# Optimization experiments

Measured on AMD Instinct MI355X. Metric: run time of the kernel, lower is better.

The kernel has to match this reference:

```python
import jax, jax.numpy as jnp
import numpy as np
import math

EPS_NORM = 1e-6
EPS_COS = 1e-6
B, L, LC = 2, 2048, 1024
D_MODEL, D_CROSS, D_HEAD = 1024, 1024, 64
N_HEADS = D_MODEL // D_HEAD


def setup_inputs() -> dict:
    key = jax.random.key(0)
    ks = jax.random.split(key, 6)
    x = jax.random.normal(ks[0], (B, L, D_MODEL), jnp.float32)
    pos = jax.random.uniform(ks[1], (B, L, 2), dtype=jnp.float32)  # normalized 2D canvas coords
    x_cross = jax.random.normal(ks[2], (B, LC, D_CROSS), jnp.float32)
    norm_scale = jnp.ones((D_MODEL,), jnp.float32)          # RMSNorm scale (init ones)
    norm_cross_scale = jnp.ones((D_CROSS,), jnp.float32)
    q_w = jax.random.normal(ks[3], (D_MODEL, D_MODEL), jnp.float32) / math.sqrt(D_MODEL)
    kv_w = jax.random.normal(ks[4], (D_CROSS, 2 * D_MODEL), jnp.float32) / math.sqrt(D_CROSS)
    # out_proj is zero-init in the original; use small random weights so the block is non-trivial
    out_w = jax.random.normal(ks[5], (D_MODEL, D_MODEL), jnp.float32) / math.sqrt(D_MODEL)
    scale = jnp.full((N_HEADS,), 10.0, jnp.float32)          # learned per-head cosine-sim scale
    # AxialRoPE2D freqs (k-diffusion style, learnable_freqs=False): [n_heads, d_head//4]
    log_min, log_max = math.log(math.pi), math.log(10.0 * math.pi)
    freqs = jnp.exp(jnp.linspace(log_min, log_max, N_HEADS * D_HEAD // 4 + 1)[:-1])
    freqs = freqs.reshape(D_HEAD // 4, N_HEADS).T            # [H, E//4]
    return dict(x=x, pos=pos, x_cross=x_cross, norm_scale=norm_scale,
                norm_cross_scale=norm_cross_scale, q_w=q_w, kv_w=kv_w,
                scale=scale, out_w=out_w, freqs=freqs)


def _rms_norm(x, scale, eps=EPS_NORM):
    ms = jnp.mean(jnp.square(x), axis=-1, keepdims=True)
    return x * (scale * jax.lax.rsqrt(ms + eps))


def reference(x, pos, x_cross, norm_scale, norm_cross_scale, q_w, kv_w, scale, out_w, freqs):
    skip = x
    xn = _rms_norm(x, norm_scale)
    xc = _rms_norm(x_cross, norm_cross_scale)
    q = xn @ q_w                                             # [B,L,D]
    kv = xc @ kv_w                                           # [B,LC,2D]
    q = q.reshape(B, L, N_HEADS, D_HEAD).transpose(0, 2, 1, 3)      # [B,H,L,E]
    kv = kv.reshape(B, LC, 2, N_HEADS, D_HEAD)               # split (t nh e), t outermost
    k = kv[:, :, 0].transpose(0, 2, 1, 3)                    # [B,H,LC,E]
    v = kv[:, :, 1].transpose(0, 2, 1, 3)
    # per-head cosine-sim QK scaling
    sq = jnp.sqrt(scale)[:, None, None]                      # [H,1,1]
    q = q * (sq * jax.lax.rsqrt(jnp.sum(jnp.square(q), -1, keepdims=True) + EPS_COS))
    k = k * (sq * jax.lax.rsqrt(jnp.sum(jnp.square(k), -1, keepdims=True) + EPS_COS))
    # axial 2D RoPE on q only (as in the original forward)
    theta = jnp.concatenate([pos[..., None, 0:1] * freqs,
                             pos[..., None, 1:2] * freqs], -1)      # [B,L,H,E//2]
    theta = jnp.moveaxis(theta, -2, -3)                      # [B,H,L,E//2]
    d = theta.shape[-1]
    q1, q2 = q[..., :d], q[..., d:]
    cos, sin = jnp.cos(theta), jnp.sin(theta)
    q = jnp.concatenate([q1 * cos - q2 * sin, q2 * cos + q1 * sin], -1)
    # SDPA with scale=1.0 (cosine-sim scaling already applied)
    attn = jax.nn.softmax(jnp.einsum('bhqe,bhke->bhqk', q, k), axis=-1)
    o = jnp.einsum('bhqk,bhke->bhqe', attn, v)
    o = o.transpose(0, 2, 1, 3).reshape(B, L, D_MODEL)       # merge heads
    return o @ out_w + skip
```

## Files before the change

kernel.cpp:

```cpp
#include <hip/hip_runtime.h>
#include <math.h>

typedef unsigned short u16;
typedef __bf16 bf16x8 __attribute__((ext_vector_type(8)));
typedef float f32x4 __attribute__((ext_vector_type(4)));

#define EPS_NORM 1e-6f
#define EPS_COS  1e-6f

static constexpr int Bc = 2;
static constexpr int Lq = 2048;
static constexpr int Lc = 1024;
static constexpr int Dm = 1024;
static constexpr int DH = 64;
static constexpr int NH = 16;

#define F32MODE(probe) ((probe)[0] == 0x3F800000u)

__device__ __forceinline__ float b2f(u16 u) {
  union { unsigned u; float f; } x; x.u = ((unsigned)u) << 16; return x.f;
}
__device__ __forceinline__ u16 f2b(float f) {
  union { float f; unsigned u; } x; x.f = f;
  unsigned v = x.u;
  v += 0x7fffu + ((v >> 16) & 1u);
  return (u16)(v >> 16);
}
__device__ __forceinline__ unsigned pkbf(float lo, float hi) {
#if __has_builtin(__builtin_amdgcn_cvt_pk_bf16_f32)
  return __builtin_bit_cast(unsigned, __builtin_amdgcn_cvt_pk_bf16_f32(lo, hi));
#else
  unsigned r;
  asm("v_cvt_pk_bf16_f32 %0, %1, %2" : "=v"(r) : "v"(lo), "v"(hi));
  return r;
#endif
}
__device__ __forceinline__ float ex2(float x) {
#if __has_builtin(__builtin_amdgcn_exp2f)
  return __builtin_amdgcn_exp2f(x);
#else
  return exp2f(x);
#endif
}
__device__ __forceinline__ float loadf(const void* p, size_t i, bool f32m) {
  return f32m ? ((const float*)p)[i] : b2f(((const u16*)p)[i]);
}
__device__ __forceinline__ void gll16(const u16* g, u16* l) {
  __builtin_amdgcn_global_load_lds(
      (const __attribute__((address_space(1))) unsigned*)g,
      (__attribute__((address_space(3))) unsigned*)l, 16, 0, 0);
}

__global__ __launch_bounds__(256) void prep_kernel(
    const void* __restrict__ qw, const void* __restrict__ kvw,
    const void* __restrict__ outw, u16* __restrict__ wqw,
    u16* __restrict__ wkvw, u16* __restrict__ woutw,
    const void* __restrict__ x, const void* __restrict__ xcr,
    const void* __restrict__ nsc, const void* __restrict__ ncs,
    u16* __restrict__ xn, u16* __restrict__ xc,
    const unsigned* __restrict__ probe) {
  bool f32m = F32MODE(probe);
  int id = blockIdx.x;
  int t = threadIdx.x;
  if (id < 6144) {
    int row = id;
    const void* src; const void* sc; u16* dst;
    if (row < Bc * Lq) { src = x; sc = nsc; dst = xn; }
    else { row -= Bc * Lq; src = xcr; sc = ncs; dst = xc; }
    float f[4]; float ss = 0.f;
    if (f32m) {
      float4 a = *(const float4*)((const float*)src + (size_t)row * Dm + t * 4);
      f[0] = a.x; f[1] = a.y; f[2] = a.z; f[3] = a.w;
    } else {
      union { uint2 u2; u16 s[4]; } v;
      v.u2 = *(const uint2*)((const u16*)src + (size_t)row * Dm + t * 4);
#pragma unroll
      for (int i = 0; i < 4; i++) f[i] = b2f(v.s[i]);
    }
#pragma unroll
    for (int i = 0; i < 4; i++) ss += f[i] * f[i];
#pragma unroll
    for (int o = 32; o > 0; o >>= 1) ss += __shfl_xor(ss, o, 64);
    __shared__ float red[4];
    if ((t & 63) == 0) red[t >> 6] = ss;
    __syncthreads();
    float inv = rsqrtf((red[0] + red[1] + red[2] + red[3]) / (float)Dm + EPS_NORM);
    union { uint2 u2; u16 s[4]; } ov;
#pragma unroll
    for (int i = 0; i < 4; i++) ov.s[i] = f2b(f[i] * loadf(sc, t * 4 + i, f32m) * inv);
    *(uint2*)(dst + (size_t)row * Dm + t * 4) = ov.u2;
  } else {
    id -= 6144;
    __shared__ u16 tile[32][33];
    const void* src; u16* dst; int N;
    if (id < 1024)      { src = qw;   dst = wqw;   N = Dm; }
    else if (id < 3072) { src = kvw;  dst = wkvw;  N = 2 * Dm; id -= 1024; }
    else                { src = outw; dst = woutw; N = Dm;     id -= 3072; }
    int k0 = (id & 31) * 32, n0 = (id >> 5) * 32;
    int tn = t & 31, tg = t >> 5;
#pragma unroll
    for (int r = 0; r < 4; r++) {
      int k = tg * 4 + r;
      tile[k][tn] = f2b(loadf(src, (size_t)(k0 + k) * N + n0 + tn, f32m));
    }
    __syncthreads();
#pragma unroll
    for (int r = 0; r < 4; r++) {
      int n = tg * 4 + r;
      dst[(size_t)(n0 + n) * Dm + k0 + tn] = tile[tn][n];
    }
  }
}

__device__ __forceinline__ void gemm_body(
    const u16* __restrict__ A, const u16* __restrict__ Bt,
    int M, int N, int m0, int n0, int mode,
    u16* __restrict__ outb, u16* __restrict__ kfp, u16* __restrict__ vt,
    const void* __restrict__ skip, void* __restrict__ Cn,
    const void* __restrict__ scale, const void* __restrict__ pos,
    const void* __restrict__ freqs, bool f32m,
    u16 (&As)[2][8192], u16 (&Bs)[2][4096]) {
  constexpr int K = Dm;
  int t = threadIdx.x;
  int wv = t >> 6, lane = t & 63;
  int r16 = lane & 15, quad = lane >> 4;

  const u16* pA[4]; const u16* pB[2]; int iLA[4], iLB[2];
#pragma unroll
  for (int c = 0; c < 4; c++) {
    int i = c * 256 + t;
    int row = i >> 3, g = (i & 7) ^ (row & 7);
    pA[c] = A + (size_t)(m0 + row) * K + g * 8;
    iLA[c] = (c * 256 + wv * 64) * 8;
  }
#pragma unroll
  for (int c = 0; c < 2; c++) {
    int i = c * 256 + t;
    int row = i >> 3, g = (i & 7) ^ (row & 7);
    pB[c] = Bt + (size_t)(n0 + row) * K + g * 8;
    iLB[c] = (c * 256 + wv * 64) * 8;
  }

  int offA[2][2], offB[2][4];
#pragma unroll
  for (int kh = 0; kh < 2; kh++) {
    int pa = ((kh * 4 + quad) ^ (r16 & 7)) * 8;
#pragma unroll
    for (int i = 0; i < 2; i++) offA[kh][i] = (wv * 32 + i * 16 + r16) * 64 + pa;
#pragma unroll
    for (int j = 0; j < 4; j++) offB[kh][j] = (j * 16 + r16) * 64 + pa;
  }

  f32x4 acc[2][4] = {};

#pragma unroll
  for (int c = 0; c < 4; c++) gll16(pA[c], &As[0][iLA[c]]);
#pragma unroll
  for (int c = 0; c < 2; c++) gll16(pB[c], &Bs[0][iLB[c]]);

  int niter = K >> 6;
  for (int it = 0; it < niter; ++it) {
    __syncthreads();
    if (it + 1 < niter) {
      int koff = (it + 1) << 6;
      int nb = (it + 1) & 1;
#pragma unroll
      for (int c = 0; c < 4; c++) gll16(pA[c] + koff, &As[nb][iLA[c]]);
#pragma unroll
      for (int c = 0; c < 2; c++) gll16(pB[c] + koff, &Bs[nb][iLB[c]]);
    }
    const u16* Ab = As[it & 1];
    const u16* Bb = Bs[it & 1];
#pragma unroll
    for (int kh = 0; kh < 2; kh++) {
      bf16x8 af[2], bf[4];
#pragma unroll
      for (int i = 0; i < 2; i++)
        af[i] = __builtin_bit_cast(bf16x8, *(const uint4*)(Ab + offA[kh][i]));
#pragma unroll
      for (int j = 0; j < 4; j++)
        bf[j] = __builtin_bit_cast(bf16x8, *(const uint4*)(Bb + offB[kh][j]));
#pragma unroll
      for (int mt = 0; mt < 2; mt++)
#pragma unroll
        for (int nt = 0; nt < 4; nt++)
          acc[mt][nt] = __builtin_amdgcn_mfma_f32_16x16x32_bf16(
              af[mt], bf[nt], acc[mt][nt], 0, 0, 0);
    }
  }

  if (mode == 2) {
#pragma unroll
    for (int mt = 0; mt < 2; mt++)
#pragma unroll
      for (int nt = 0; nt < 4; nt++)
#pragma unroll
        for (int r = 0; r < 4; r++) {
          int m = m0 + wv * 32 + mt * 16 + quad * 4 + r;
          int n = n0 + nt * 16 + r16;
          size_t idx = (size_t)m * N + n;
          float v = acc[mt][nt][r] + loadf(skip, idx, f32m);
          if (f32m) ((float*)Cn)[idx] = v;
          else      outb[idx] = f2b(v);
        }
    return;
  }

  if (mode == 1 && n0 >= Dm) {
    int hh = (n0 - Dm) >> 6;
#pragma unroll
    for (int mt = 0; mt < 2; mt++)
#pragma unroll
      for (int r = 0; r < 4; r++) {
        int m = m0 + wv * 32 + mt * 16 + quad * 4 + r;
        int bb = m >> 10, lc = m & (Lc - 1);
        u16* tb = vt + ((size_t)(bb * NH + hh) * 16 + (lc >> 6)) * 4096;
        int kin = lc & 63;
#pragma unroll
        for (int nt = 0; nt < 4; nt++) {
          int d = nt * 16 + r16;
          tb[d * 64 + ((kin >> 3) ^ (d & 7)) * 8 + (kin & 7)] = f2b(acc[mt][nt][r]);
        }
      }
    return;
  }

  int hh = (n0 & (Dm - 1)) >> 6;
  float sqs = sqrtf(loadf(scale, hh, f32m));
  float fr = (mode == 0) ? loadf(freqs, hh * 16 + r16, f32m) : 0.f;
#pragma unroll
  for (int mt = 0; mt < 2; mt++) {
    float ss[4];
#pragma unroll
    for (int r = 0; r < 4; r++) {
      ss[r] = 0.f;
#pragma unroll
      for (int nt = 0; nt < 4; nt++) ss[r] += acc[mt][nt][r] * acc[mt][nt][r];
    }
#pragma unroll
    for (int o = 1; o < 16; o <<= 1)
#pragma unroll
      for (int r = 0; r < 4; r++) ss[r] += __shfl_xor(ss[r], o, 64);
#pragma unroll
    for (int r = 0; r < 4; r++) {
      int m = m0 + wv * 32 + mt * 16 + quad * 4 + r;
      float inv = sqs * rsqrtf(ss[r] + EPS_COS);
      if (mode == 1) {
        int bb = m >> 10, lc = m & (Lc - 1);
        size_t base = ((size_t)((bb * NH + hh) * Lc) + lc) * 64;
#pragma unroll
        for (int nt = 0; nt < 4; nt++)
          kfp[base + nt * 16 + r16] = f2b(acc[mt][nt][r] * inv);
      } else {
        int bb = m >> 11, l = m & (Lq - 1);
        float p0 = loadf(pos, (size_t)m * 2 + 0, f32m);
        float p1 = loadf(pos, (size_t)m * 2 + 1, f32m);
        size_t base = ((size_t)((bb * NH + hh) * Lq) + l) * 64;
#pragma unroll
        for (int nt = 0; nt < 2; nt++) {
          float th = (nt ? p1 : p0) * fr;
          float c, s;
          sincosf(th, &s, &c);
          float lo = acc[mt][nt][r] * inv, hi = acc[mt][nt + 2][r] * inv;
          outb[base + nt * 16 + r16]       = f2b(lo * c - hi * s);
          outb[base + (nt + 2) * 16 + r16] = f2b(hi * c + lo * s);
        }
      }
    }
  }
}

__global__ __launch_bounds__(256) void qkv_gemm_kernel(
    const u16* __restrict__ xn, const u16* __restrict__ wqw,
    const u16* __restrict__ xc, const u16* __restrict__ wkvw,
    u16* __restrict__ qf, u16* __restrict__ kf, u16* __restrict__ vt,
    const void* __restrict__ scale, const void* __restrict__ pos,
    const void* __restrict__ freqs, const unsigned* __restrict__ probe) {
  __shared__ u16 As[2][8192];
  __shared__ u16 Bs[2][4096];
  bool f32m = F32MODE(probe);
  int blk = blockIdx.x;
  if (blk < 512) {
    gemm_body(xn, wqw, Bc * Lq, Dm, (blk >> 4) * 128, (blk & 15) * 64, 0,
              qf, nullptr, nullptr, nullptr, nullptr, scale, pos, freqs,
              f32m, As, Bs);
  } else {
    int id = blk - 512;
    gemm_body(xc, wkvw, Bc * Lc, 2 * Dm, (id >> 5) * 128, (id & 31) * 64, 1,
              nullptr, kf, vt, nullptr, nullptr, scale, nullptr, nullptr,
              f32m, As, Bs);
  }
}

__global__ __launch_bounds__(256) void final_gemm_kernel(
    const u16* __restrict__ ob, const u16* __restrict__ woutw,
    const void* __restrict__ skip, void* __restrict__ Cn,
    u16* __restrict__ outb, const unsigned* __restrict__ probe) {
  __shared__ u16 As[2][8192];
  __shared__ u16 Bs[2][4096];
  bool f32m = F32MODE(probe);
  int blk = blockIdx.x;
  gemm_body(ob, woutw, Bc * Lq, Dm, (blk >> 4) * 128, (blk & 15) * 64, 2,
            outb, nullptr, nullptr, skip, Cn, nullptr, nullptr, nullptr,
            f32m, As, Bs);
}

__global__ __launch_bounds__(256) void attn_kernel(
    const u16* __restrict__ qf, const u16* __restrict__ kf,
    const u16* __restrict__ vt, u16* __restrict__ o_out,
    const void* __restrict__ scale, const unsigned* __restrict__ probe) {
  __shared__ u16 Kt[2][4096];
  __shared__ u16 Vs[2][4096];
  __shared__ u16 Pl[4][1024];

  int blk = blockIdx.x;
  int bh = blk & 31;
  int qt = blk >> 5;
  int h = bh & 15;
  bool f32m = F32MODE(probe);
  const float L2E = 1.44269504089f;
  float sh = loadf(scale, h, f32m);
  float shb = sh * L2E;
  const u16* kbase = kf + (size_t)bh * Lc * DH;
  const u16* vtb   = vt + (size_t)bh * 16 * 4096;
  int t = threadIdx.x;
  int wv = t >> 6, lane = t & 63;
  int r16 = lane & 15, quad = lane >> 4;

  const u16* qb0 = qf + ((size_t)bh * Lq + qt * 64 + wv * 16) * DH;
  bf16x8 af00 = __builtin_bit_cast(bf16x8, *(const uint4*)(qb0 + r16 * DH + 0  + quad * 8));
  bf16x8 af01 = __builtin_bit_cast(bf16x8, *(const uint4*)(qb0 + r16 * DH + 32 + quad * 8));

  int e0 = t, e1 = 256 + t;
  int row0 = e0 >> 3, g0 = (e0 & 7) ^ (row0 & 7);
  int row1 = e1 >> 3, g1 = (e1 & 7) ^ (row1 & 7);
  const u16* pK0 = kbase + (size_t)row0 * DH + g0 * 8;
  const u16* pK1 = kbase + (size_t)row1 * DH + g1 * 8;
  const u16* pV0 = vtb + e0 * 8;
  const u16* pV1 = vtb + e1 * 8;
  int iS0 = (wv * 64) * 8, iS1 = (256 + wv * 64) * 8;
  int kphys0 = ((quad)     ^ (r16 & 7)) * 8;
  int kphys1 = ((4 | quad) ^ (r16 & 7)) * 8;

  int poff[4][4];
#pragma unroll
  for (int r = 0; r < 4; r++) {
    int mrow = quad * 4 + r;
    int bx = mrow & 7;
    int base = mrow * 64 + (r16 & 7);
    int c0 = r16 >> 3;
    poff[r][0] = base + ((c0    ) ^ bx) * 8;
    poff[r][1] = base + ((c0 + 2) ^ bx) * 8;
    poff[r][2] = base + ((c0 + 4) ^ bx) * 8;
    poff[r][3] = base + ((c0 + 6) ^ bx) * 8;
  }

  float l0[4] = {0.f, 0.f, 0.f, 0.f};
  f32x4 oa0[4] = {{0,0,0,0},{0,0,0,0},{0,0,0,0},{0,0,0,0}};

  gll16(pK0, &Kt[0][iS0]); gll16(pK1, &Kt[0][iS1]);
  gll16(pV0, &Vs[0][iS0]); gll16(pV1, &Vs[0][iS1]);

  for (int it = 0; it < Lc / 64; ++it) {
    __syncthreads();
    if (it + 1 < Lc / 64) {
      size_t koff = (size_t)(it + 1) * 64 * DH;
      size_t voff = (size_t)(it + 1) * 4096;
      int nb = (it + 1) & 1;
      gll16(pK0 + koff, &Kt[nb][iS0]);
      gll16(pK1 + koff, &Kt[nb][iS1]);
      gll16(pV0 + voff, &Vs[nb][iS0]);
      gll16(pV1 + voff, &Vs[nb][iS1]);
    }
    const u16* Kb = Kt[it & 1];
    const u16* Vb = Vs[it & 1];

    f32x4 s0[4];
#pragma unroll
    for (int nt = 0; nt < 4; nt++) {
      int nrow = (nt * 16 + r16) * 64;
      bf16x8 bf0 = __builtin_bit_cast(bf16x8, *(const uint4*)(Kb + nrow + kphys0));
      bf16x8 bf1 = __builtin_bit_cast(bf16x8, *(const uint4*)(Kb + nrow + kphys1));
      s0[nt] = (f32x4){0.f, 0.f, 0.f, 0.f};
      s0[nt] = __builtin_amdgcn_mfma_f32_16x16x32_bf16(af00, bf0, s0[nt], 0, 0, 0);
      s0[nt] = __builtin_amdgcn_mfma_f32_16x16x32_bf16(af01, bf1, s0[nt], 0, 0, 0);
    }

    {
      u16* P = &Pl[wv][0];
#pragma unroll
      for (int r = 0; r < 4; r++) {
        float p0 = ex2(fmaf(s0[0][r], L2E, -shb));
        float p1 = ex2(fmaf(s0[1][r], L2E, -shb));
        float p2 = ex2(fmaf(s0[2][r], L2E, -shb));
        float p3 = ex2(fmaf(s0[3][r], L2E, -shb));
        l0[r] += (p0 + p1) + (p2 + p3);
        unsigned pa = pkbf(p0, p1), pb = pkbf(p2, p3);
        P[poff[r][0]] = (u16)pa;
        P[poff[r][1]] = (u16)(pa >> 16);
        P[poff[r][2]] = (u16)pb;
        P[poff[r][3]] = (u16)(pb >> 16);
      }
    }

#pragma unroll
    for (int dt = 0; dt < 4; dt++) {
      int vrow = (dt * 16 + r16) * 64;
#pragma unroll
      for (int kc = 0; kc < 2; kc++) {
        int ph = kc ? kphys1 : kphys0;
        bf16x8 bu  = __builtin_bit_cast(bf16x8, *(const uint4*)(Vb + vrow + ph));
        bf16x8 au0 = __builtin_bit_cast(bf16x8, *(const uint4*)&Pl[wv][r16 * 64 + ph]);
        oa0[dt] = __builtin_amdgcn_mfma_f32_16x16x32_bf16(au0, bu, oa0[dt], 0, 0, 0);
      }
    }
  }

  int b = bh >> 4;
  float inv[4];
#pragma unroll
  for (int r = 0; r < 4; r++) {
    float l = l0[r];
#pragma unroll
    for (int o = 8; o > 0; o >>= 1) l += __shfl_xor(l, o, 64);
    inv[r] = 1.f / l;
  }
#pragma unroll
  for (int dt = 0; dt < 4; dt++)
#pragma unroll
    for (int r = 0; r < 4; r++) {
      int m = qt * 64 + wv * 16 + quad * 4 + r;
      o_out[((size_t)(b * Lq + m)) * Dm + h * DH + dt * 16 + r16] =
          f2b(oa0[dt][r] * inv[r]);
    }
}

extern "C" void kernel_launch(void* const* d_in, const int* in_sizes, int n_in,
                              void* d_out, int out_size, void* d_ws, size_t ws_size,
                              hipStream_t stream) {
  const void* x     = d_in[0];
  const void* pos   = d_in[1];
  const void* xcr   = d_in[2];
  const void* nsc   = d_in[3];
  const void* ncs   = d_in[4];
  const void* qw    = d_in[5];
  const void* kvw   = d_in[6];
  const void* scale = d_in[7];
  const void* outw  = d_in[8];
  const void* freqs = d_in[9];
  const unsigned* probe = (const unsigned*)nsc;

  char* ws = (char*)d_ws;
  const size_t MB = 1u << 20;
  u16*   wqw  = (u16*)(ws + 0 * MB);
  u16*   wkvw = (u16*)(ws + 2 * MB);
  u16*   woutw= (u16*)(ws + 6 * MB);
  u16*   xn   = (u16*)(ws + 8 * MB);
  u16*   ob   = (u16*)(ws + 8 * MB);
  u16*   xc   = (u16*)(ws + 16 * MB);
  u16*   qf   = (u16*)(ws + 20 * MB);
  u16*   kf   = (u16*)(ws + 28 * MB);
  u16*   vt   = (u16*)(ws + 32 * MB);

  prep_kernel<<<6144 + 4096, 256, 0, stream>>>(
      qw, kvw, outw, wqw, wkvw, woutw, x, xcr, nsc, ncs, xn, xc, probe);
  qkv_gemm_kernel<<<1024, 256, 0, stream>>>(xn, wqw, xc, wkvw, qf, kf, vt,
                                            scale, pos, freqs, probe);
  attn_kernel<<<1024, 256, 0, stream>>>(qf, kf, vt, ob, scale, probe);
  final_gemm_kernel<<<512, 256, 0, stream>>>(ob, woutw, x, d_out, (u16*)d_out, probe);
}
```

Before: 195.1 us.

## Keep attention probabilities in registers via transposed S MFMA and K row permutation

Computes S^T by swapping MFMA operands so that each lane already holds the probability values in the A-operand layout needed by the PV MFMA. This removes the per-wave LDS scratch buffer and its scattered 16-bit stores and reloads. K rows are permuted at load time so that the register-held P columns line up with the V layout. The row-sum reduction moves to a cross-quad shuffle followed by a broadcast, and correctness depends on the permutation exactly matching the MFMA fragment layout.

```diff
diff --git a/kernel.cpp b/kernel.cpp
--- a/kernel.cpp
+++ b/kernel.cpp
@@ -311,7 +311,6 @@
     const void* __restrict__ scale, const unsigned* __restrict__ probe) {
   __shared__ u16 Kt[2][4096];
   __shared__ u16 Vs[2][4096];
-  __shared__ u16 Pl[4][1024];
 
   int blk = blockIdx.x;
   int bh = blk & 31;
@@ -332,30 +331,19 @@
   bf16x8 af01 = __builtin_bit_cast(bf16x8, *(const uint4*)(qb0 + r16 * DH + 32 + quad * 8));
 
   int e0 = t, e1 = 256 + t;
-  int row0 = e0 >> 3, g0 = (e0 & 7) ^ (row0 & 7);
-  int row1 = e1 >> 3, g1 = (e1 & 7) ^ (row1 & 7);
-  const u16* pK0 = kbase + (size_t)row0 * DH + g0 * 8;
-  const u16* pK1 = kbase + (size_t)row1 * DH + g1 * 8;
+  int rho0 = e0 >> 3, g0 = (e0 & 7) ^ (rho0 & 7);
+  int rho1 = e1 >> 3, g1 = (e1 & 7) ^ (rho1 & 7);
+  int gk0 = ((rho0 & 28) << 1) | ((rho0 & 32) >> 3) | (rho0 & 3);
+  int gk1 = ((rho1 & 28) << 1) | ((rho1 & 32) >> 3) | (rho1 & 3);
+  const u16* pK0 = kbase + (size_t)gk0 * DH + g0 * 8;
+  const u16* pK1 = kbase + (size_t)gk1 * DH + g1 * 8;
   const u16* pV0 = vtb + e0 * 8;
   const u16* pV1 = vtb + e1 * 8;
   int iS0 = (wv * 64) * 8, iS1 = (256 + wv * 64) * 8;
   int kphys0 = ((quad)     ^ (r16 & 7)) * 8;
   int kphys1 = ((4 | quad) ^ (r16 & 7)) * 8;
 
-  int poff[4][4];
-#pragma unroll
-  for (int r = 0; r < 4; r++) {
-    int mrow = quad * 4 + r;
-    int bx = mrow & 7;
-    int base = mrow * 64 + (r16 & 7);
-    int c0 = r16 >> 3;
-    poff[r][0] = base + ((c0    ) ^ bx) * 8;
-    poff[r][1] = base + ((c0 + 2) ^ bx) * 8;
-    poff[r][2] = base + ((c0 + 4) ^ bx) * 8;
-    poff[r][3] = base + ((c0 + 6) ^ bx) * 8;
-  }
-
-  float l0[4] = {0.f, 0.f, 0.f, 0.f};
+  float lacc = 0.f;
   f32x4 oa0[4] = {{0,0,0,0},{0,0,0,0},{0,0,0,0},{0,0,0,0}};
 
   gll16(pK0, &Kt[0][iS0]); gll16(pK1, &Kt[0][iS1]);
@@ -375,56 +363,53 @@
     const u16* Kb = Kt[it & 1];
     const u16* Vb = Vs[it & 1];
 
-    f32x4 s0[4];
+    f32x4 sT[4];
 #pragma unroll
     for (int nt = 0; nt < 4; nt++) {
       int nrow = (nt * 16 + r16) * 64;
       bf16x8 bf0 = __builtin_bit_cast(bf16x8, *(const uint4*)(Kb + nrow + kphys0));
       bf16x8 bf1 = __builtin_bit_cast(bf16x8, *(const uint4*)(Kb + nrow + kphys1));
-      s0[nt] = (f32x4){0.f, 0.f, 0.f, 0.f};
-      s0[nt] = __builtin_amdgcn_mfma_f32_16x16x32_bf16(af00, bf0, s0[nt], 0, 0, 0);
-      s0[nt] = __builtin_amdgcn_mfma_f32_16x16x32_bf16(af01, bf1, s0[nt], 0, 0, 0);
-    }
-
-    {
-      u16* P = &Pl[wv][0];
-#pragma unroll
-      for (int r = 0; r < 4; r++) {
-        float p0 = ex2(fmaf(s0[0][r], L2E, -shb));
-        float p1 = ex2(fmaf(s0[1][r], L2E, -shb));
-        float p2 = ex2(fmaf(s0[2][r], L2E, -shb));
-        float p3 = ex2(fmaf(s0[3][r], L2E, -shb));
-        l0[r] += (p0 + p1) + (p2 + p3);
-        unsigned pa = pkbf(p0, p1), pb = pkbf(p2, p3);
-        P[poff[r][0]] = (u16)pa;
-        P[poff[r][1]] = (u16)(pa >> 16);
-        P[poff[r][2]] = (u16)pb;
-        P[poff[r][3]] = (u16)(pb >> 16);
-      }
-    }
+      sT[nt] = (f32x4){0.f, 0.f, 0.f, 0.f};
+      sT[nt] = __builtin_amdgcn_mfma_f32_16x16x32_bf16(bf0, af00, sT[nt], 0, 0, 0);
+      sT[nt] = __builtin_amdgcn_mfma_f32_16x16x32_bf16(bf1, af01, sT[nt], 0, 0, 0);
+    }
+
+    float p[4][4];
+#pragma unroll
+    for (int nt = 0; nt < 4; nt++)
+#pragma unroll
+      for (int r = 0; r < 4; r++)
+        p[nt][r] = ex2(fmaf(sT[nt][r], L2E, -shb));
+#pragma unroll
+    for (int nt = 0; nt < 4; nt++)
+      lacc += (p[nt][0] + p[nt][1]) + (p[nt][2] + p[nt][3]);
+
+    uint4 u0, u1;
+    u0.x = pkbf(p[0][0], p[0][1]); u0.y = pkbf(p[0][2], p[0][3]);
+    u0.z = pkbf(p[2][0], p[2][1]); u0.w = pkbf(p[2][2], p[2][3]);
+    u1.x = pkbf(p[1][0], p[1][1]); u1.y = pkbf(p[1][2], p[1][3]);
+    u1.z = pkbf(p[3][0], p[3][1]); u1.w = pkbf(p[3][2], p[3][3]);
+    bf16x8 pa0 = __builtin_bit_cast(bf16x8, u0);
+    bf16x8 pa1 = __builtin_bit_cast(bf16x8, u1);
 
 #pragma unroll
     for (int dt = 0; dt < 4; dt++) {
       int vrow = (dt * 16 + r16) * 64;
-#pragma unroll
-      for (int kc = 0; kc < 2; kc++) {
-        int ph = kc ? kphys1 : kphys0;
-        bf16x8 bu  = __builtin_bit_cast(bf16x8, *(const uint4*)(Vb + vrow + ph));
-        bf16x8 au0 = __builtin_bit_cast(bf16x8, *(const uint4*)&Pl[wv][r16 * 64 + ph]);
-        oa0[dt] = __builtin_amdgcn_mfma_f32_16x16x32_bf16(au0, bu, oa0[dt], 0, 0, 0);
-      }
-    }
-  }
+      bf16x8 bu0 = __builtin_bit_cast(bf16x8, *(const uint4*)(Vb + vrow + kphys0));
+      bf16x8 bu1 = __builtin_bit_cast(bf16x8, *(const uint4*)(Vb + vrow + kphys1));
+      oa0[dt] = __builtin_amdgcn_mfma_f32_16x16x32_bf16(pa0, bu0, oa0[dt], 0, 0, 0);
+      oa0[dt] = __builtin_amdgcn_mfma_f32_16x16x32_bf16(pa1, bu1, oa0[dt], 0, 0, 0);
+    }
+  }
+
+  lacc += __shfl_xor(lacc, 16, 64);
+  lacc += __shfl_xor(lacc, 32, 64);
+  float inv[4];
+#pragma unroll
+  for (int r = 0; r < 4; r++)
+    inv[r] = 1.f / __shfl(lacc, quad * 4 + r, 64);
 
   int b = bh >> 4;
-  float inv[4];
-#pragma unroll
-  for (int r = 0; r < 4; r++) {
-    float l = l0[r];
-#pragma unroll
-    for (int o = 8; o > 0; o >>= 1) l += __shfl_xor(l, o, 64);
-    inv[r] = 1.f / l;
-  }
 #pragma unroll
   for (int dt = 0; dt < 4; dt++)
 #pragma unroll
```

After: 199.0 us. About the same (+2.0%).
